# Kernel optimization log

Hardware: AMD Instinct MI355X
Metric: run time of the kernel (lower is better)

## Reference

```python
import jax, jax.numpy as jnp
import numpy as np
from jax import lax

ULB_LEN = 50000  # hardcoded ulb_dest_len in Cluster.__init__
EPS = 1e-8       # torch.cosine_similarity eps


def _l2norm(x):
    n = jnp.sqrt(jnp.sum(x * x, axis=-1, keepdims=True))
    return x / jnp.maximum(n, EPS)


def setup_inputs() -> dict:
    key = jax.random.key(0)
    k1, k2, k3, k4, k5 = jax.random.split(key, 5)
    B, C, D, K = 32768, 1000, 256, 16
    return {
        "feature": jax.random.normal(k1, (B, D), dtype=jnp.float32),
        "pred": jax.random.normal(k2, (B, C), dtype=jnp.float32),
        "centroids": jax.random.normal(k3, (C, D), dtype=jnp.float32),
        "pred_top_N": jax.random.uniform(k4, (C, K), dtype=jnp.float32),
        "unlabeled_index": jax.random.randint(k5, (B,), 0, ULB_LEN, dtype=jnp.int64),
    }


def reference(feature, pred, centroids, pred_top_N, unlabeled_index):
    B = feature.shape[0]
    C, K = pred_top_N.shape

    # batched cosine similarity to centroids -> argmax label, max cos
    cos = _l2norm(feature) @ _l2norm(centroids).T          # [B, C]
    label = jnp.argmax(cos, axis=1)                        # [B]
    cos_f = jnp.max(cos, axis=1)                           # [B]

    # confidence scores from softmax(pred)
    scores = jnp.max(jax.nn.softmax(pred, axis=1), axis=1)  # [B]

    # per-class mean / unbiased variance of cos_f (torch.var default unbiased)
    ones = jnp.ones((B,), dtype=cos_f.dtype)
    cnt = jax.ops.segment_sum(ones, label, num_segments=C)
    s1 = jax.ops.segment_sum(cos_f, label, num_segments=C)
    s2 = jax.ops.segment_sum(cos_f * cos_f, label, num_segments=C)
    mean = s1 / jnp.maximum(cnt, 1.0)
    var = (s2 - cnt * mean * mean) / jnp.maximum(cnt - 1.0, 1.0)
    std = jnp.sqrt(jnp.maximum(var, 0.0) + 1e-12)

    # weight[i] = normal(mean, std).pdf(cos_f[i]) if cos_f[i] < mean[label] else 1
    m_i, s_i = mean[label], std[label]
    inv_sqrt_2pi = 1.0 / jnp.sqrt(2.0 * jnp.pi).astype(cos_f.dtype)
    pdf = jnp.exp(-0.5 * ((cos_f - m_i) / s_i) ** 2) * inv_sqrt_2pi / s_i
    weight = jnp.where(cos_f < m_i, pdf, jnp.ones_like(cos_f))

    # sequential top-N scatter-insert into pred_top_N / fake_index
    fake_index = jnp.full((C, K), -1, dtype=jnp.int32)

    def step(carry, xs):
        topN, fidx = carry
        lb, sc, ui = xs
        row = topN[lb]                       # [K]
        mi = jnp.argmin(row)
        mv = row[mi]
        do = sc > mv
        topN = topN.at[lb, mi].set(jnp.where(do, sc, mv))
        fidx = fidx.at[lb, mi].set(jnp.where(do, ui.astype(jnp.int32), fidx[lb, mi]))
        return (topN, fidx), None

    (topN, fidx), _ = lax.scan(
        step, (pred_top_N, fake_index),
        (label, scores, unlabeled_index))

    # selected_label scatter (all samples selected: select==1 everywhere)
    selected_label = jnp.full((ULB_LEN,), -1, dtype=jnp.int32)
    selected_label = selected_label.at[unlabeled_index].set(label.astype(jnp.int32))

    return label.astype(jnp.float32), weight, topN, fidx, selected_label
```

## Files before the change

### kernel.cpp

```cpp
#include <hip/hip_runtime.h>
#include <cstdint>
#include <cstddef>

#define B_N   32768
#define C_N   1000
#define C_PAD 1024
#define D_N   256
#define K_N   16
#define ULB_N 50000
#define NCHUNK 128
#define CAP_L 128

#define OFF_L 0
#define OFF_W 32768
#define OFF_T 65536
#define OFF_F 81536
#define OFF_S 97536

typedef __attribute__((ext_vector_type(8))) short short8;
typedef __attribute__((ext_vector_type(4))) float f32x4;

__device__ __forceinline__ unsigned ordf(float f) {
  unsigned u = __float_as_uint(f);
  return (u & 0x80000000u) ? ~u : (u | 0x80000000u);
}
__device__ __forceinline__ float iordf(unsigned h) {
  unsigned u = (h & 0x80000000u) ? (h & 0x7FFFFFFFu) : ~h;
  return __uint_as_float(u);
}
__device__ __forceinline__ unsigned short f2bf(float f) {
  unsigned u = __float_as_uint(f);
  return (unsigned short)((u + 0x7FFFu + ((u >> 16) & 1u)) >> 16);
}
__device__ __forceinline__ float bf2f(unsigned short h) {
  return __uint_as_float(((unsigned)h) << 16);
}

__device__ __forceinline__ void pack_body(const float* __restrict__ src,
                                          short8* __restrict__ dst,
                                          int mtL, int mt0, int nreal) {
  __shared__ float s[16][260];
  __shared__ float part[16][16];
  __shared__ float dv[16];
  const int t = threadIdx.x;
  const int r = t >> 4, c4 = (t & 15) * 4;
  const int grow = (mt0 + mtL) * 16 + r;
  #pragma unroll
  for (int i = 0; i < 4; ++i) {
    float4 v;
    if (grow < nreal) v = *reinterpret_cast<const float4*>(&src[(size_t)grow * D_N + c4 + 64 * i]);
    else { v.x = 0.f; v.y = 0.f; v.z = 0.f; v.w = 0.f; }
    s[r][c4 + 64 * i + 0] = v.x; s[r][c4 + 64 * i + 1] = v.y;
    s[r][c4 + 64 * i + 2] = v.z; s[r][c4 + 64 * i + 3] = v.w;
  }
  __syncthreads();
  {
    int c0 = t & 15;
    float ss = 0.f;
    #pragma unroll
    for (int j = 0; j < 16; ++j) { float x = s[r][c0 + 16 * j]; ss += x * x; }
    part[r][c0] = ss;
  }
  __syncthreads();
  if (t < 16) {
    float ss = 0.f;
    #pragma unroll
    for (int j = 0; j < 16; ++j) ss += part[t][j];
    dv[t] = 1.0f / fmaxf(sqrtf(ss), 1e-8f);
  }
  __syncthreads();
  #pragma unroll
  for (int i = 0; i < 4; ++i) {
    int p = t + 256 * i;
    int si = p >> 6, l = p & 63;
    int mr = l & 15, g = l >> 4;
    int kc = (si & 7) * 32 + g * 8;
    bool lo = si >= 8;
    float di = dv[mr];
    short8 v;
    #pragma unroll
    for (int j = 0; j < 8; ++j) {
      float q = s[mr][kc + j] * di;
      unsigned short hi = f2bf(q);
      unsigned short e = lo ? f2bf(q - bf2f(hi)) : hi;
      v[j] = (short)e;
    }
    dst[(size_t)mtL * 1024 + p] = v;
  }
}

__global__ __launch_bounds__(256) void k_front(const float* __restrict__ cent,
                                               const float* __restrict__ pred,
                                               short8* __restrict__ Bp,
                                               float* __restrict__ scores,
                                               unsigned long long* keys, float* s1, float* s2,
                                               int* cnt, int* besti) {
  __shared__ float red[8];
  int i = blockIdx.x * blockDim.x + threadIdx.x;
  if (i < B_N)  keys[i] = 0ull;
  if (i < C_PAD) { s1[i] = 0.f; s2[i] = 0.f; cnt[i] = 0; }
  if (i < ULB_N) besti[i] = -1;
  if (blockIdx.x < 64) pack_body(cent, Bp, blockIdx.x, 0, C_N);

  int r = blockIdx.x, t = threadIdx.x;
  const float* row = pred + (size_t)r * C_N;
  float4 v;
  bool act = t < 250;
  if (act) v = *reinterpret_cast<const float4*>(&row[t * 4]);
  else { v.x = -INFINITY; v.y = -INFINITY; v.z = -INFINITY; v.w = -INFINITY; }
  float m = fmaxf(fmaxf(v.x, v.y), fmaxf(v.z, v.w));
  #pragma unroll
  for (int mk = 1; mk < 64; mk <<= 1) m = fmaxf(m, __shfl_xor(m, mk, 64));
  int wid = t >> 6, lane = t & 63;
  if (lane == 0) red[wid] = m;
  __syncthreads();
  m = fmaxf(fmaxf(red[0], red[1]), fmaxf(red[2], red[3]));
  float s = act ? expf(v.x - m) + expf(v.y - m) + expf(v.z - m) + expf(v.w - m) : 0.f;
  #pragma unroll
  for (int mk = 1; mk < 64; mk <<= 1) s += __shfl_xor(s, mk, 64);
  __syncthreads();
  if (lane == 0) red[4 + wid] = s;
  __syncthreads();
  if (t == 0) {
    float S = ((red[4] + red[5]) + red[6]) + red[7];
    scores[r] = 1.0f / S;
  }
}

__global__ __launch_bounds__(256) void k_pack(const float* __restrict__ src,
                                              short8* __restrict__ dst,
                                              int mt0, int nreal) {
  pack_body(src, dst, blockIdx.x, mt0, nreal);
}

__global__ __launch_bounds__(256, 2) void k_mfma(const short8* __restrict__ Ap,
                                                 const short8* __restrict__ Bp,
                                                 unsigned long long* __restrict__ keys,
                                                 int row0) {
  const int bid = blockIdx.x;
  const int nby = gridDim.x >> 3;
  int byl, bx;
  if ((nby & 63) == 0) {
    int xcd = bid & 7, j = bid >> 3;
    int slab = nby >> 3;
    int grp = j >> 6, jj = j & 63;
    byl = xcd * slab + grp * 8 + (jj & 7);
    bx = jj >> 3;
  } else { byl = bid >> 3; bx = bid & 7; }

  const int w = threadIdx.x >> 6, l = threadIdx.x & 63;
  const int wm = (w & 1) * 64, wn = (w >> 1) * 64;
  const short8* a0 = Ap + (size_t)(byl * 8 + (wm >> 4)) * 1024 + l;
  const short8* b0 = Bp + (size_t)(bx * 8 + (wn >> 4)) * 1024 + l;

  f32x4 acc[4][4];
  #pragma unroll
  for (int i = 0; i < 4; ++i)
    #pragma unroll
    for (int j = 0; j < 4; ++j) { acc[i][j][0] = 0.f; acc[i][j][1] = 0.f; acc[i][j][2] = 0.f; acc[i][j][3] = 0.f; }

  short8 A0h[4], B0h[4], A0l[4], B0l[4];
  short8 A1h[4], B1h[4], A1l[4], B1l[4];
#define LOADSET(Xh, Yh, Xl, Yl, ks) { \
    _Pragma("unroll") \
    for (int i = 0; i < 4; ++i) Xh[i] = a0[(ks) * 64 + i * 1024]; \
    _Pragma("unroll") \
    for (int i = 0; i < 4; ++i) Yh[i] = b0[(ks) * 64 + i * 1024]; \
    _Pragma("unroll") \
    for (int i = 0; i < 4; ++i) Xl[i] = a0[((ks) + 8) * 64 + i * 1024]; \
    _Pragma("unroll") \
    for (int i = 0; i < 4; ++i) Yl[i] = b0[((ks) + 8) * 64 + i * 1024]; }
#define MFMA16(fa, fb) { \
    _Pragma("unroll") \
    for (int mi = 0; mi < 4; ++mi) \
      _Pragma("unroll") \
      for (int nj = 0; nj < 4; ++nj) \
        acc[mi][nj] = __builtin_amdgcn_mfma_f32_16x16x32_bf16(fa[mi], fb[nj], acc[mi][nj], 0, 0, 0); }
#define MFMA48(Xh, Yh, Xl, Yl) { MFMA16(Xh, Yh) MFMA16(Xl, Yh) MFMA16(Xh, Yl) }
#define FENCE __builtin_amdgcn_sched_barrier(0);

  LOADSET(A0h, B0h, A0l, B0l, 0)
  #pragma unroll 1
  for (int ks = 0; ks < 6; ks += 2) {
    LOADSET(A1h, B1h, A1l, B1l, ks + 1)
    FENCE
    MFMA48(A0h, B0h, A0l, B0l)
    FENCE
    LOADSET(A0h, B0h, A0l, B0l, ks + 2)
    FENCE
    MFMA48(A1h, B1h, A1l, B1l)
    FENCE
  }
  LOADSET(A1h, B1h, A1l, B1l, 7)
  FENCE
  MFMA48(A0h, B0h, A0l, B0l)
  FENCE
  MFMA48(A1h, B1h, A1l, B1l)
#undef LOADSET
#undef MFMA16
#undef MFMA48
#undef FENCE

  const int cb = bx * 128 + wn + (l & 15);
  #pragma unroll
  for (int mi = 0; mi < 4; ++mi) {
    #pragma unroll
    for (int r = 0; r < 4; ++r) {
      float bv = -INFINITY; int bc = 0x7FFFFFFF;
      #pragma unroll
      for (int nj = 0; nj < 4; ++nj) {
        int c = cb + nj * 16;
        float v = acc[mi][nj][r];
        if (c < C_N && v > bv) { bv = v; bc = c; }
      }
      #pragma unroll
      for (int mk = 1; mk < 16; mk <<= 1) {
        float ov = __shfl_xor(bv, mk, 64);
        int oc = __shfl_xor(bc, mk, 64);
        if (ov > bv || (ov == bv && oc < bc)) { bv = ov; bc = oc; }
      }
      if ((l & 15) == 0) {
        unsigned long long kk =
            (((unsigned long long)ordf(bv)) << 32) |
            (unsigned long long)(0xFFFFFFFFu - (unsigned)bc);
        atomicMax(&keys[row0 + byl * 128 + wm + mi * 16 + (l >> 4) * 4 + r], kk);
      }
    }
  }
}

__global__ __launch_bounds__(256) void k_post(const unsigned long long* __restrict__ keys,
                                              const int* __restrict__ ui,
                                              int* __restrict__ labels, float* __restrict__ cosf_,
                                              float* __restrict__ s1, float* __restrict__ s2,
                                              int* __restrict__ cnt, int* __restrict__ besti,
                                              unsigned short* __restrict__ lrank,
                                              unsigned short* __restrict__ hist,
                                              float* __restrict__ out) {
  __shared__ int lab[256];
  __shared__ unsigned histl[C_PAD];
  int chunk = blockIdx.x, t = threadIdx.x;
  int b = chunk * 256 + t;
  #pragma unroll
  for (int r = 0; r < 4; ++r) histl[t + 256 * r] = 0;
  unsigned long long k = keys[b];
  int c = (int)(0xFFFFFFFFu - (unsigned)k);
  float f = iordf((unsigned)(k >> 32));
  labels[b] = c;
  cosf_[b] = f;
  out[OFF_L + b] = (float)c;
  atomicAdd(&s1[c], f);
  atomicAdd(&s2[c], f * f);
  atomicAdd(&cnt[c], 1);
  atomicMax(&besti[ui[b]], b);
  lab[t] = c;
  __syncthreads();
  atomicAdd(&histl[c], 1u);
  unsigned rk = 0;
  for (int j = 0; j < t; ++j) rk += (lab[j] == c);
  lrank[b] = (unsigned short)rk;
  __syncthreads();
  #pragma unroll
  for (int r = 0; r < 4; ++r)
    hist[chunk * C_PAD + t + 256 * r] = (unsigned short)histl[t + 256 * r];
}

__global__ __launch_bounds__(256) void k_prefix(const unsigned short* __restrict__ hist,
                                                unsigned short* __restrict__ base,
                                                int* __restrict__ class_n) {
  int c = blockIdx.x * 4 + (threadIdx.x >> 6);
  int l = threadIdx.x & 63;
  unsigned h0 = hist[(2 * l) * C_PAD + c];
  unsigned h1 = hist[(2 * l + 1) * C_PAD + c];
  unsigned pair = h0 + h1;
  unsigned s = pair;
  #pragma unroll
  for (int off = 1; off < 64; off <<= 1) {
    unsigned v = __shfl_up(s, off, 64);
    if (l >= off) s += v;
  }
  unsigned excl = s - pair;
  base[(2 * l) * C_PAD + c] = (unsigned short)excl;
  base[(2 * l + 1) * C_PAD + c] = (unsigned short)(excl + h0);
  if (l == 63) class_n[c] = (int)s;
}

__global__ __launch_bounds__(256) void k_sw(const int* __restrict__ labels,
                                            const unsigned short* __restrict__ lrank,
                                            const unsigned short* __restrict__ base,
                                            const float* __restrict__ scores,
                                            const int* __restrict__ ui,
                                            const float* __restrict__ cosf_,
                                            const float* __restrict__ s1,
                                            const float* __restrict__ s2,
                                            const int* __restrict__ cnt,
                                            const int* __restrict__ besti,
                                            float* __restrict__ lists_s,
                                            int* __restrict__ lists_u,
                                            float* __restrict__ out) {
  int b = blockIdx.x * blockDim.x + threadIdx.x;
  if (b >= B_N) return;
  int c = labels[b];
  int chunk = b >> 8;
  int pos = (int)base[chunk * C_PAD + c] + (int)lrank[b];
  if (pos < CAP_L) {
    lists_s[c * CAP_L + pos] = scores[b];
    lists_u[c * CAP_L + pos] = ui[b];
  }
  float n = (float)cnt[c];
  float m = s1[c] / fmaxf(n, 1.0f);
  float var = (s2[c] - n * m * m) / fmaxf(n - 1.0f, 1.0f);
  float sd = sqrtf(fmaxf(var, 0.0f) + 1e-12f);
  float cf = cosf_[b];
  float wgt = 1.0f;
  if (cf < m) {
    float z = (cf - m) / sd;
    const float inv = 0.3989422804014327f;
    wgt = expf(-0.5f * (z * z)) * inv / sd;
  }
  out[OFF_W + b] = wgt;
  {
    int bi = besti[b];
    out[OFF_S + b] = (bi < 0) ? -1.0f : (float)labels[bi];
  }
  int p2 = b + B_N;
  if (p2 < ULB_N) {
    int bi = besti[p2];
    out[OFF_S + p2] = (bi < 0) ? -1.0f : (float)labels[bi];
  }
}

__global__ __launch_bounds__(256) void k_replay(const float* __restrict__ ptn,
                                                const float* __restrict__ lists_s,
                                                const int* __restrict__ lists_u,
                                                const int* __restrict__ class_n,
                                                const int* __restrict__ labels,
                                                const float* __restrict__ scores,
                                                const int* __restrict__ ui,
                                                float* __restrict__ out) {
  int c = blockIdx.x * 4 + (threadIdx.x >> 6);
  int lane = threadIdx.x & 63;
  if (c >= C_N) return;

  float tv[K_N]; int fi[K_N];
  #pragma unroll
  for (int j = 0; j < K_N; ++j) { tv[j] = ptn[c * K_N + j]; fi[j] = -1; }

  auto ins = [&](float s, int u) {
    float mv = tv[0]; int mi = 0;
    #pragma unroll
    for (int j = 1; j < K_N; ++j) { if (tv[j] < mv) { mv = tv[j]; mi = j; } }
    if (s > mv) {
      #pragma unroll
      for (int j = 0; j < K_N; ++j) { if (j == mi) { tv[j] = s; fi[j] = u; } }
    }
  };

  int n = class_n[c];
  if (n <= CAP_L) {
    for (int t0 = 0; t0 < n; t0 += 64) {
      float s = 0.f; int u = 0;
      int idx = t0 + lane;
      if (idx < n) { s = lists_s[c * CAP_L + idx]; u = lists_u[c * CAP_L + idx]; }
      int lim = min(64, n - t0);
      for (int t = 0; t < lim; ++t) {
        float ss = __shfl(s, t, 64);
        int uu = __shfl(u, t, 64);
        ins(ss, uu);
      }
    }
  } else {
    for (int t0 = 0; t0 < B_N; t0 += 64) {
      int lb = labels[t0 + lane];
      unsigned long long match = __ballot(lb == c);
      while (match) {
        int t = __ffsll((long long)match) - 1;
        match &= match - 1;
        int b = t0 + t;
        ins(scores[b], ui[b]);
      }
    }
  }

  if (lane == 0) {
    #pragma unroll
    for (int j = 0; j < K_N; ++j) {
      out[OFF_T + c * K_N + j] = tv[j];
      out[OFF_F + c * K_N + j] = (float)fi[j];
    }
  }
}

extern "C" void kernel_launch(void* const* d_in, const int* in_sizes, int n_in,
                              void* d_out, int out_size, void* d_ws, size_t ws_size,
                              hipStream_t stream) {
  const float* feat = (const float*)d_in[0];
  const float* pred = (const float*)d_in[1];
  const float* cent = (const float*)d_in[2];
  const float* ptn  = (const float*)d_in[3];
  const int*   ui   = (const int*)d_in[4];
  float* out = (float*)d_out;
  char* ws = (char*)d_ws;

  size_t o = 0;
  auto alloc = [&](size_t bytes) { void* p = ws + o; o += (bytes + 255) & ~size_t(255); return p; };
  short8* Bp                = (short8*)alloc(64 * 1024 * 16);
  unsigned long long* keys  = (unsigned long long*)alloc(B_N * 8);
  int*   labels             = (int*)  alloc(B_N * 4);
  float* scores             = (float*)alloc(B_N * 4);
  float* cosf_              = (float*)alloc(B_N * 4);
  float* s1                 = (float*)alloc(C_PAD * 4);
  float* s2                 = (float*)alloc(C_PAD * 4);
  int*   cnt                = (int*)  alloc(C_PAD * 4);
  int*   besti              = (int*)  alloc(ULB_N * 4);
  unsigned short* lrank     = (unsigned short*)alloc(B_N * 2);
  unsigned short* hist      = (unsigned short*)alloc(NCHUNK * C_PAD * 2);
  unsigned short* base      = (unsigned short*)alloc(NCHUNK * C_PAD * 2);
  int*   class_n            = (int*)  alloc(C_PAD * 4);
  float* lists_s            = (float*)alloc(C_N * CAP_L * 4);
  int*   lists_u            = (int*)  alloc(C_N * CAP_L * 4);

  size_t avail = (ws_size > o) ? ws_size - o : 0;
  int g128 = (int)(avail / 131072ull);
  if (g128 < 1) g128 = 1;
  if (g128 > 256) g128 = 256;
  if (g128 >= 64) g128 &= ~63;
  else if (g128 >= 8) g128 &= ~7;
  short8* Achunk = (short8*)(ws + o);

  k_front    <<<B_N, 256, 0, stream>>>(cent, pred, Bp, scores, keys, s1, s2, cnt, besti);
  for (int c0 = 0; c0 < 256; c0 += g128) {
    int g = (g128 < 256 - c0) ? g128 : (256 - c0);
    k_pack   <<<g * 8, 256, 0, stream>>>(feat, Achunk, c0 * 8, B_N);
    k_mfma   <<<g * 8, 256, 0, stream>>>(Achunk, Bp, keys, c0 * 128);
  }
  k_post     <<<NCHUNK, 256, 0, stream>>>(keys, ui, labels, cosf_, s1, s2, cnt, besti, lrank, hist, out);
  k_prefix   <<<256, 256, 0, stream>>>(hist, base, class_n);
  k_sw       <<<B_N / 256, 256, 0, stream>>>(labels, lrank, base, scores, ui, cosf_, s1, s2, cnt, besti, lists_s, lists_u, out);
  k_replay   <<<250, 256, 0, stream>>>(ptn, lists_s, lists_u, class_n, labels, scores, ui, out);
}
```

Measured before the change: 150.6 us.

## Halve MFMA block N-tile to 64 and drop register double-buffering for occupancy

The bf16 MFMA similarity kernel now has each block compute a 128x64 output tile instead of 128x128. The grid doubles and the XCD swizzle is adjusted to match. Each wave keeps a 4x2 accumulator grid, and the explicit two-stage register prefetch with sched barriers is replaced by a simple load-then-compute loop. The launch bound rises to 4 blocks per CU. The aim is more waves per CU to hide load latency, at the cost of more A-tile reloads and no software pipelining.

Measured after the change: 176.0 us. +16.9%, slower.

```diff
diff --git a/kernel.cpp b/kernel.cpp
--- a/kernel.cpp
+++ b/kernel.cpp
@@ -133,82 +133,65 @@
   pack_body(src, dst, blockIdx.x, mt0, nreal);
 }
 
-__global__ __launch_bounds__(256, 2) void k_mfma(const short8* __restrict__ Ap,
+__global__ __launch_bounds__(256, 4) void k_mfma(const short8* __restrict__ Ap,
                                                  const short8* __restrict__ Bp,
                                                  unsigned long long* __restrict__ keys,
                                                  int row0) {
   const int bid = blockIdx.x;
-  const int nby = gridDim.x >> 3;
+  const int nby = gridDim.x >> 4;
   int byl, bx;
   if ((nby & 63) == 0) {
     int xcd = bid & 7, j = bid >> 3;
     int slab = nby >> 3;
-    int grp = j >> 6, jj = j & 63;
+    int grp = j >> 7, jj = j & 127;
     byl = xcd * slab + grp * 8 + (jj & 7);
     bx = jj >> 3;
-  } else { byl = bid >> 3; bx = bid & 7; }
+  } else { byl = bid >> 4; bx = bid & 15; }
 
   const int w = threadIdx.x >> 6, l = threadIdx.x & 63;
-  const int wm = (w & 1) * 64, wn = (w >> 1) * 64;
+  const int wm = (w & 1) * 64;
+  const int wn = (w >> 1) * 32;
   const short8* a0 = Ap + (size_t)(byl * 8 + (wm >> 4)) * 1024 + l;
-  const short8* b0 = Bp + (size_t)(bx * 8 + (wn >> 4)) * 1024 + l;
-
-  f32x4 acc[4][4];
+  const short8* b0 = Bp + (size_t)(bx * 4 + (wn >> 4)) * 1024 + l;
+
+  f32x4 acc[4][2];
   #pragma unroll
   for (int i = 0; i < 4; ++i)
     #pragma unroll
-    for (int j = 0; j < 4; ++j) { acc[i][j][0] = 0.f; acc[i][j][1] = 0.f; acc[i][j][2] = 0.f; acc[i][j][3] = 0.f; }
-
-  short8 A0h[4], B0h[4], A0l[4], B0l[4];
-  short8 A1h[4], B1h[4], A1l[4], B1l[4];
-#define LOADSET(Xh, Yh, Xl, Yl, ks) { \
-    _Pragma("unroll") \
-    for (int i = 0; i < 4; ++i) Xh[i] = a0[(ks) * 64 + i * 1024]; \
-    _Pragma("unroll") \
-    for (int i = 0; i < 4; ++i) Yh[i] = b0[(ks) * 64 + i * 1024]; \
-    _Pragma("unroll") \
-    for (int i = 0; i < 4; ++i) Xl[i] = a0[((ks) + 8) * 64 + i * 1024]; \
-    _Pragma("unroll") \
-    for (int i = 0; i < 4; ++i) Yl[i] = b0[((ks) + 8) * 64 + i * 1024]; }
-#define MFMA16(fa, fb) { \
+    for (int j = 0; j < 2; ++j) { acc[i][j][0] = 0.f; acc[i][j][1] = 0.f; acc[i][j][2] = 0.f; acc[i][j][3] = 0.f; }
+
+  short8 Ah[4], Al[4], Bh[2], Bl[2];
+#define MFMA8(fa, fb) { \
     _Pragma("unroll") \
     for (int mi = 0; mi < 4; ++mi) \
       _Pragma("unroll") \
-      for (int nj = 0; nj < 4; ++nj) \
+      for (int nj = 0; nj < 2; ++nj) \
         acc[mi][nj] = __builtin_amdgcn_mfma_f32_16x16x32_bf16(fa[mi], fb[nj], acc[mi][nj], 0, 0, 0); }
-#define MFMA48(Xh, Yh, Xl, Yl) { MFMA16(Xh, Yh) MFMA16(Xl, Yh) MFMA16(Xh, Yl) }
-#define FENCE __builtin_amdgcn_sched_barrier(0);
-
-  LOADSET(A0h, B0h, A0l, B0l, 0)
+
   #pragma unroll 1
-  for (int ks = 0; ks < 6; ks += 2) {
-    LOADSET(A1h, B1h, A1l, B1l, ks + 1)
-    FENCE
-    MFMA48(A0h, B0h, A0l, B0l)
-    FENCE
-    LOADSET(A0h, B0h, A0l, B0l, ks + 2)
-    FENCE
-    MFMA48(A1h, B1h, A1l, B1l)
-    FENCE
-  }
-  LOADSET(A1h, B1h, A1l, B1l, 7)
-  FENCE
-  MFMA48(A0h, B0h, A0l, B0l)
-  FENCE
-  MFMA48(A1h, B1h, A1l, B1l)
-#undef LOADSET
-#undef MFMA16
-#undef MFMA48
-#undef FENCE
-
-  const int cb = bx * 128 + wn + (l & 15);
+  for (int ks = 0; ks < 8; ++ks) {
+    #pragma unroll
+    for (int i = 0; i < 4; ++i) Ah[i] = a0[ks * 64 + i * 1024];
+    #pragma unroll
+    for (int i = 0; i < 2; ++i) Bh[i] = b0[ks * 64 + i * 1024];
+    #pragma unroll
+    for (int i = 0; i < 4; ++i) Al[i] = a0[(ks + 8) * 64 + i * 1024];
+    #pragma unroll
+    for (int i = 0; i < 2; ++i) Bl[i] = b0[(ks + 8) * 64 + i * 1024];
+    MFMA8(Ah, Bh)
+    MFMA8(Al, Bh)
+    MFMA8(Ah, Bl)
+  }
+#undef MFMA8
+
+  const int cb = bx * 64 + wn + (l & 15);
   #pragma unroll
   for (int mi = 0; mi < 4; ++mi) {
     #pragma unroll
     for (int r = 0; r < 4; ++r) {
       float bv = -INFINITY; int bc = 0x7FFFFFFF;
       #pragma unroll
-      for (int nj = 0; nj < 4; ++nj) {
+      for (int nj = 0; nj < 2; ++nj) {
         int c = cb + nj * 16;
         float v = acc[mi][nj][r];
         if (c < C_N && v > bv) { bv = v; bc = c; }
@@ -432,7 +415,7 @@
   for (int c0 = 0; c0 < 256; c0 += g128) {
     int g = (g128 < 256 - c0) ? g128 : (256 - c0);
     k_pack   <<<g * 8, 256, 0, stream>>>(feat, Achunk, c0 * 8, B_N);
-    k_mfma   <<<g * 8, 256, 0, stream>>>(Achunk, Bp, keys, c0 * 128);
+    k_mfma   <<<g * 16, 256, 0, stream>>>(Achunk, Bp, keys, c0 * 128);
   }
   k_post     <<<NCHUNK, 256, 0, stream>>>(keys, ui, labels, cosf_, s1, s2, cnt, besti, lrank, hist, out);
   k_prefix   <<<256, 256, 0, stream>>>(hist, base, class_n);
```
